# Performance work log

Measured on AMD Instinct MI355X. Metric: run time of the kernel, lower is better.

Reference implementation:

```python
import jax, jax.numpy as jnp
import numpy as np

N, IN_DIM, E, H, L, M = 65536, 512, 128, 4, 2, 256
DH = E // H  # 32

def _gaussian_orthogonal(m, d, rng):
    # FAVOR+ gaussian orthogonal random matrix (performer_pytorch, scaling=0)
    blocks = []
    for _ in range((m + d - 1) // d):
        q, _ = np.linalg.qr(rng.normal(size=(d, d)))
        blocks.append(q.T)
    mat = np.concatenate(blocks)[:m]
    mult = np.linalg.norm(rng.normal(size=(m, d)), axis=1)
    return (mult[:, None] * mat).astype(np.float32)

def setup_inputs() -> dict:
    rng = np.random.default_rng(0)
    r = lambda *s: jnp.asarray(rng.normal(size=s, scale=0.02), jnp.float32)
    z = lambda *s: jnp.zeros(s, jnp.float32)
    o = lambda *s: jnp.ones(s, jnp.float32)
    return dict(
        x=jnp.asarray(rng.normal(size=(N, IN_DIM)), dtype=jnp.float32),
        Wpin=r(IN_DIM, E), bpin=z(E),
        lag=o(L, E), lab=z(L, E),                    # performer inner pre-LN (attn)
        Wq=r(L, E, E), Wk=r(L, E, E), Wv=r(L, E, E), # qkv (no bias in performer_pytorch)
        Wo=r(L, E, E), bo=z(L, E),                   # attn to_out
        lbg=o(L, E), lbb=z(L, E),                    # performer inner pre-LN (ff)
        Wf1=r(L, E, 4 * E), bf1=z(L, 4 * E),         # performer inner GELU FFN
        Wf2=r(L, 4 * E, E), bf2=z(L, E),
        Wpo=r(L, E, E), bpo=z(L, E),                 # PerformerSelfAttention.out_proj
        n1g=o(L, E), n1b=z(L, E),                    # block norm1
        Wn1=r(L, E, 4 * E), bn1=z(L, 4 * E),         # block ReLU FFN
        Wn2=r(L, 4 * E, E), bn2=z(L, E),
        n2g=o(L, E), n2b=z(L, E),                    # block norm2
        Wc=r(E, 1), bc=z(1),                         # classifier
        proj=jnp.stack([jnp.asarray(_gaussian_orthogonal(M, DH, rng)) for _ in range(L)]),
    )

def _ln(x, g, b, eps=1e-5):
    mu = x.mean(-1, keepdims=True)
    var = ((x - mu) ** 2).mean(-1, keepdims=True)
    return (x - mu) * jax.lax.rsqrt(var + eps) * g + b

def _softmax_kernel(data, proj, is_query, eps=1e-4):
    # data: [1,H,N,DH]; proj: [M,DH]  (performer_pytorch softmax_kernel)
    dn = data.shape[-1] ** -0.25
    ratio = proj.shape[0] ** -0.5
    dd = jnp.einsum('bhnd,md->bhnm', data * dn, proj)
    diag = (data ** 2).sum(-1, keepdims=True) * 0.5 * (dn * dn)
    stab = jnp.max(dd, -1, keepdims=True) if is_query else jnp.max(dd)
    return ratio * (jnp.exp(dd - diag - stab) + eps)

def _linear_attn(qf, kf, v):
    # non-causal FAVOR+: O(N*M*DH)
    D = jnp.einsum('bhnm,bhm->bhn', qf, kf.sum(-2))          # denominator
    ctx = jnp.einsum('bhnm,bhnd->bhmd', kf, v)               # [1,H,M,DH]
    return jnp.einsum('bhnm,bhmd->bhnd', qf, ctx) / D[..., None]

def _forward(x, Wpin, bpin, lag, lab, Wq, Wk, Wv, Wo, bo, lbg, lbb,
             Wf1, bf1, Wf2, bf2, Wpo, bpo, n1g, n1b, Wn1, bn1, Wn2, bn2,
             n2g, n2b, Wc, bc, proj):
    h = (x @ Wpin + bpin)[None]  # [1,N,E]
    split = lambda t: t.reshape(1, -1, H, DH).transpose(0, 2, 1, 3)
    for l in range(L):
        # --- inner Performer (depth=1): pre-LN attn + pre-LN GELU FFN, residuals ---
        y = _ln(h, lag[l], lab[l])
        q, k, v = split(y @ Wq[l]), split(y @ Wk[l]), split(y @ Wv[l])
        qf = _softmax_kernel(q, proj[l], True)
        kf = _softmax_kernel(k, proj[l], False)
        a = _linear_attn(qf, kf, v).transpose(0, 2, 1, 3).reshape(1, -1, E)
        h1 = h + (a @ Wo[l] + bo[l])
        y2 = _ln(h1, lbg[l], lbb[l])
        h2 = h1 + (jax.nn.gelu(y2 @ Wf1[l] + bf1[l], approximate=False) @ Wf2[l] + bf2[l])
        # --- outer block: post-LN residual attn + post-LN ReLU FFN ---
        attn_out = h2 @ Wpo[l] + bpo[l]
        h = _ln(h + attn_out, n1g[l], n1b[l])
        ffn = jax.nn.relu(h @ Wn1[l] + bn1[l]) @ Wn2[l] + bn2[l]
        h = _ln(h + ffn, n2g[l], n2b[l])
    return jax.nn.sigmoid(h[0] @ Wc + bc)[:, 0]  # [N]

def reference(x, Wpin, bpin, lag, lab, Wq, Wk, Wv, Wo, bo, lbg, lbb,
              Wf1, bf1, Wf2, bf2, Wpo, bpo, n1g, n1b, Wn1, bn1, Wn2, bn2,
              n2g, n2b, Wc, bc, proj):
    return _forward(x, Wpin, bpin, lag, lab, Wq, Wk, Wv, Wo, bo, lbg, lbb,
                    Wf1, bf1, Wf2, bf2, Wpo, bpo, n1g, n1b, Wn1, bn1, Wn2, bn2,
                    n2g, n2b, Wc, bc, proj)
```

## Files before the change

kernel.cpp:

```cpp
#include <hip/hip_runtime.h>
#include <math.h>

#define NTOK  65536
#define EDIM  128
#define HN    4
#define DHD   32
#define MF    256
#define LLAYERS 2
#define INDIM 512
#define FDIM  512
#define CR    512
#define NCHK  (NTOK/CR)

#define DN    0.4204482076268573f
#define DN2   0.17677669529663687f
#define KEPS  1e-4f

typedef unsigned short u16;
typedef unsigned int   u32;
typedef __attribute__((ext_vector_type(8))) __bf16 bf16x8;
typedef __attribute__((ext_vector_type(4))) float  f32x4;

__device__ __forceinline__ u16 f2bf(float f){
  u32 u = __float_as_uint(f);
  u32 r = (u + 0x7fffu + ((u >> 16) & 1u)) >> 16;
  return (u16)r;
}
__device__ __forceinline__ float bf2f(u16 h){ return __uint_as_float(((u32)h) << 16); }

__device__ __forceinline__ void gload_lds16(const void* g, void* l){
  __builtin_amdgcn_global_load_lds(
      (const __attribute__((address_space(1))) u32*)g,
      (__attribute__((address_space(3))) u32*)l, 16, 0, 0);
}

__device__ __forceinline__ unsigned f2ord(float f){
  unsigned u = __float_as_uint(f);
  return (u & 0x80000000u) ? ~u : (u | 0x80000000u);
}
__device__ __forceinline__ float ord2f(unsigned e){
  unsigned u = (e & 0x80000000u) ? (e & 0x7fffffffu) : ~e;
  return __uint_as_float(u);
}

struct PrepArgs {
  const float* Wpin; const float* Wq; const float* Wk; const float* Wv;
  const float* Wo;   const float* Wpo; const float* Wf1; const float* Wf2;
  const float* Wn1;  const float* Wn2; const float* proj;
};

__global__ __launch_bounds__(256) void prep_kernel(PrepArgs a, u16* __restrict__ wts,
                                                   u16* __restrict__ pjb,
                                                   unsigned* __restrict__ stabp)
{
  int idx = blockIdx.x * 256 + threadIdx.x;
  if (idx == 0) { stabp[0] = 0x007FFFFFu; stabp[1] = 0x007FFFFFu; }
  const float* sp; u16* dp; int r, K, J;
  if      (idx <  65536) { sp = a.Wpin; dp = wts;          r = idx;          K = 512; J = 128; }
  else if (idx <  98304) { sp = a.Wq;   dp = wts +  65536; r = idx -  65536; K = 128; J = 128; }
  else if (idx < 131072) { sp = a.Wk;   dp = wts +  98304; r = idx -  98304; K = 128; J = 128; }
  else if (idx < 163840) { sp = a.Wv;   dp = wts + 131072; r = idx - 131072; K = 128; J = 128; }
  else if (idx < 196608) { sp = a.Wo;   dp = wts + 163840; r = idx - 163840; K = 128; J = 128; }
  else if (idx < 229376) { sp = a.Wpo;  dp = wts + 196608; r = idx - 196608; K = 128; J = 128; }
  else if (idx < 360448) { sp = a.Wf1;  dp = wts + 229376; r = idx - 229376; K = 128; J = 512; }
  else if (idx < 491520) { sp = a.Wf2;  dp = wts + 360448; r = idx - 360448; K = 512; J = 128; }
  else if (idx < 622592) { sp = a.Wn1;  dp = wts + 491520; r = idx - 491520; K = 128; J = 512; }
  else if (idx < 753664) { sp = a.Wn2;  dp = wts + 622592; r = idx - 622592; K = 512; J = 128; }
  else { int p = idx - 753664; pjb[p] = f2bf(a.proj[p] * DN); return; }
  int kj = K * J;
  int l = r / kj, rr = r - l * kj;
  int j = rr / K, k = rr - j * K;
  dp[r] = f2bf(sp[(size_t)l * kj + (size_t)k * J + j]);
}

template<int LNM, bool A32, bool MULTI>
__global__ __launch_bounds__(256, 4) void gemm_f(
    const u16* __restrict__ A, const float* __restrict__ Af,
    const u16* __restrict__ Bt,
    const float* __restrict__ bias, const u16* __restrict__ res,
    u16* __restrict__ outRaw, int K, int J, int op,
    const float* __restrict__ g1, const float* __restrict__ b1, u16* __restrict__ outL1,
    u16* __restrict__ outAux,
    const float* __restrict__ Wcp, const float* __restrict__ bcp, float* __restrict__ outCls)
{
  __shared__ __align__(16) u16 pool[18432];
  __shared__ float lnred[2][2][32][2];
  u16* Al = pool;
  u16* Bl = pool + 6144;
  const int tid  = threadIdx.x;
  const int lane = tid & 63;
  const int w    = tid >> 6;
  const int wr   = w >> 1, wc = w & 1;
  const int bid  = blockIdx.x;
  const int nwg8 = gridDim.x >> 3;
  const int bsw  = (bid & 7) * nwg8 + (bid >> 3);
  const int n0   = bsw * 64;
  const int jb   = MULTI ? 0 : blockIdx.y * 128;
  const u16* Bu  = MULTI ? (Bt + (size_t)blockIdx.y * 32768) : Bt;

  f32x4 acc[2][4];
#pragma unroll
  for (int m = 0; m < 2; ++m)
#pragma unroll
    for (int n = 0; n < 4; ++n) acc[m][n] = (f32x4){0.f, 0.f, 0.f, 0.f};

  const int srow = lane >> 2;
  const int skg  = (lane & 3) ^ ((lane >> 3) & 3);

  auto stageB = [&](int buf, int k0) {
#pragma unroll
    for (int i = 0; i < 2; ++i) {
      const int rb = 2 * w + i;
      gload_lds16(Bu + (size_t)(jb + rb * 16 + srow) * K + k0 + skg * 8,
                  &Bl[buf * 4096 + rb * 512]);
    }
  };
  auto stageA16 = [&](int buf, int k0) {
    gload_lds16(A + (size_t)(n0 + w * 16 + srow) * K + k0 + skg * 8,
                &Al[buf * 2048 + w * 512]);
  };

  const int r16f = lane & 15;
  const int kgl  = (lane >> 4) ^ ((lane >> 1) & 3);
  const int foff = r16f * 32 + kgl * 8;

  auto compute = [&](int cur) {
    bf16x8 af[2], bfg[4];
#pragma unroll
    for (int m = 0; m < 2; ++m)
      af[m]  = *reinterpret_cast<const bf16x8*>(&Al[cur * 2048 + (wr * 2 + m) * 512 + foff]);
#pragma unroll
    for (int n = 0; n < 4; ++n)
      bfg[n] = *reinterpret_cast<const bf16x8*>(&Bl[cur * 4096 + (wc * 4 + n) * 512 + foff]);
#pragma unroll
    for (int m = 0; m < 2; ++m)
#pragma unroll
      for (int n = 0; n < 4; ++n)
        acc[m][n] = __builtin_amdgcn_mfma_f32_16x16x32_bf16(af[m], bfg[n], acc[m][n], 0, 0, 0);
  };

  if constexpr (A32) {
    constexpr int T = 16;
    float4 fA[3][2];
    const int r = tid >> 2, hf = tid & 3;
    auto loadA = [&](int slot, int k0) {
      const float* gp = Af + (size_t)(n0 + r) * 512 + k0 + hf * 8;
      fA[slot][0] = ((const float4*)gp)[0];
      fA[slot][1] = ((const float4*)gp)[1];
    };
    const int rbA = r >> 4, r16A = r & 15, swzA = (r16A >> 1) & 3;
    auto writeA = [&](int slot, int buf) {
      uint4 p0;
      p0.x = (u32)f2bf(fA[slot][0].x) | ((u32)f2bf(fA[slot][0].y) << 16);
      p0.y = (u32)f2bf(fA[slot][0].z) | ((u32)f2bf(fA[slot][0].w) << 16);
      p0.z = (u32)f2bf(fA[slot][1].x) | ((u32)f2bf(fA[slot][1].y) << 16);
      p0.w = (u32)f2bf(fA[slot][1].z) | ((u32)f2bf(fA[slot][1].w) << 16);
      *reinterpret_cast<uint4*>(&Al[buf * 2048 + rbA * 512 + r16A * 32 + (hf ^ swzA) * 8]) = p0;
    };
    loadA(0, 0); loadA(1, 32); loadA(2, 64);
    stageB(0, 0); stageB(1, 32);
    asm volatile("s_waitcnt vmcnt(8)" ::: "memory");
    writeA(0, 0);
#pragma unroll
    for (int t = 0; t < T; ++t) {
      if (t + 2 < T) asm volatile("s_waitcnt vmcnt(4) lgkmcnt(0)" ::: "memory");
      else           asm volatile("s_waitcnt vmcnt(0) lgkmcnt(0)" ::: "memory");
      __builtin_amdgcn_s_barrier();
      if (t + 1 < T) writeA((t + 1) % 3, (t + 1) % 3);
      if (t + 3 < T) loadA((t + 3) % 3, (t + 3) * 32);
      if (t + 2 < T) stageB((t + 2) % 3, (t + 2) * 32);
      compute(t % 3);
    }
    __builtin_amdgcn_s_barrier();
  } else {
    const int T = K >> 5;
    stageA16(0, 0); stageB(0, 0);
    stageA16(1, 32); stageB(1, 32);
    for (int t = 0; t < T; ++t) {
      if (t + 1 < T) asm volatile("s_waitcnt vmcnt(3) lgkmcnt(0)" ::: "memory");
      else           asm volatile("s_waitcnt vmcnt(0) lgkmcnt(0)" ::: "memory");
      __builtin_amdgcn_s_barrier();
      int cur = t % 3;
      if (t + 2 < T) { stageA16((t + 2) % 3, (t + 2) * 32); stageB((t + 2) % 3, (t + 2) * 32); }
      compute(cur);
    }
    __builtin_amdgcn_s_barrier();
  }

  const int colb = jb + wc * 64 + (lane & 15);
  const int rowb = n0 + wr * 32 + (lane >> 4) * 4;
  float bv[4];
#pragma unroll
  for (int n = 0; n < 4; ++n) bv[n] = bias ? bias[colb + n * 16] : 0.f;

  float v[2][4][4];
#pragma unroll
  for (int m = 0; m < 2; ++m)
#pragma unroll
    for (int n = 0; n < 4; ++n)
#pragma unroll
      for (int j = 0; j < 4; ++j) {
        float t = acc[m][n][j] + bv[n];
        if (res) t += bf2f(res[(size_t)(rowb + m * 16 + j) * J + colb + n * 16]);
        v[m][n][j] = t;
      }

  if constexpr (MULTI) {
    if (blockIdx.y == 2) {
      u16* tb = pool;
#pragma unroll
      for (int m = 0; m < 2; ++m)
#pragma unroll
        for (int n = 0; n < 4; ++n)
#pragma unroll
          for (int j = 0; j < 4; ++j)
            tb[(wc * 64 + n * 16 + (lane & 15)) * 72 + wr * 32 + m * 16 + (lane >> 4) * 4 + j]
                = f2bf(v[m][n][j]);
      __syncthreads();
      { const int c2 = tid >> 1, hf2 = tid & 1;
        const uint4* src = reinterpret_cast<const uint4*>(&tb[c2 * 72 + hf2 * 32]);
        uint4* dst = reinterpret_cast<uint4*>(outAux + (size_t)c2 * NTOK + n0 + hf2 * 32);
        dst[0] = src[0]; dst[1] = src[1]; dst[2] = src[2]; dst[3] = src[3]; }
      return;
    }
    u16* out0 = (blockIdx.y == 0) ? outRaw : outL1;
#pragma unroll
    for (int m = 0; m < 2; ++m)
#pragma unroll
      for (int n = 0; n < 4; ++n)
#pragma unroll
        for (int j = 0; j < 4; ++j)
          out0[(size_t)(rowb + m * 16 + j) * J + colb + n * 16] = f2bf(v[m][n][j]);
    return;
  }

  if (outRaw) {
#pragma unroll
    for (int m = 0; m < 2; ++m)
#pragma unroll
      for (int n = 0; n < 4; ++n)
#pragma unroll
        for (int j = 0; j < 4; ++j)
          outRaw[(size_t)(rowb + m * 16 + j) * J + colb + n * 16] = f2bf(v[m][n][j]);
  }

  if constexpr (LNM > 0 && !MULTI) {
    float rs[2][4], rq[2][4];
#pragma unroll
    for (int m = 0; m < 2; ++m)
#pragma unroll
      for (int j = 0; j < 4; ++j) {
        float s = 0.f, q = 0.f;
#pragma unroll
        for (int n = 0; n < 4; ++n) { float t = v[m][n][j]; s += t; q += t * t; }
        rs[m][j] = s; rq[m][j] = q;
      }
#pragma unroll
    for (int o = 1; o < 16; o <<= 1)
#pragma unroll
      for (int m = 0; m < 2; ++m)
#pragma unroll
        for (int j = 0; j < 4; ++j) {
          rs[m][j] += __shfl_xor(rs[m][j], o);
          rq[m][j] += __shfl_xor(rq[m][j], o);
        }
    __syncthreads();
    if ((lane & 15) == 0) {
#pragma unroll
      for (int m = 0; m < 2; ++m)
#pragma unroll
        for (int j = 0; j < 4; ++j) {
          int rloc = m * 16 + (lane >> 4) * 4 + j;
          lnred[wr][wc][rloc][0] = rs[m][j];
          lnred[wr][wc][rloc][1] = rq[m][j];
        }
    }
    __syncthreads();
    float gg[4], bb[4];
#pragma unroll
    for (int n = 0; n < 4; ++n) { gg[n] = g1[colb + n * 16]; bb[n] = b1[colb + n * 16]; }
#pragma unroll
    for (int m = 0; m < 2; ++m)
#pragma unroll
      for (int j = 0; j < 4; ++j) {
        int rloc = m * 16 + (lane >> 4) * 4 + j;
        float ts = rs[m][j] + lnred[wr][wc ^ 1][rloc][0];
        float tq = rq[m][j] + lnred[wr][wc ^ 1][rloc][1];
        float mu = ts * (1.f / 128.f);
        float rsig = rsqrtf(tq * (1.f / 128.f) - mu * mu + 1e-5f);
#pragma unroll
        for (int n = 0; n < 4; ++n)
          v[m][n][j] = (v[m][n][j] - mu) * rsig * gg[n] + bb[n];
      }
    if (outL1) {
#pragma unroll
      for (int m = 0; m < 2; ++m)
#pragma unroll
        for (int n = 0; n < 4; ++n)
#pragma unroll
          for (int j = 0; j < 4; ++j)
            outL1[(size_t)(rowb + m * 16 + j) * J + colb + n * 16] = f2bf(v[m][n][j]);
    }
  }
}

template<bool RESPOST, int ACT, int LNM>
__global__ __launch_bounds__(256, 2) void mega_f(
    const u16* __restrict__ A0, const u16* __restrict__ W0t,
    const float* __restrict__ b0p, const u16* __restrict__ res0,
    const float* __restrict__ g0, const float* __restrict__ bg0,
    const u16* __restrict__ W1t, const float* __restrict__ fb1p,
    const u16* __restrict__ W2t, const float* __restrict__ fb2p,
    u16* __restrict__ out,
    const float* __restrict__ g1, const float* __restrict__ bt1,
    u16* __restrict__ outL2, const float* __restrict__ g2, const float* __restrict__ bt2,
    const float* __restrict__ Wcp, const float* __restrict__ bcp, float* __restrict__ outCls)
{
  __shared__ __align__(16) u16 As[4][2048];
  __shared__ __align__(16) u16 Hs[4][2048];
  __shared__ __align__(16) u16 Bs[3][4096];
  __shared__ float lnred[2][2][32][2];
  const int tid  = threadIdx.x;
  const int lane = tid & 63;
  const int w    = tid >> 6;
  const int wr   = w >> 1, wc = w & 1;
  const int bid  = blockIdx.x;
  const int bsw  = (bid & 7) * (gridDim.x >> 3) + (bid >> 3);
  const int n0   = bsw * 64;

  const int srow = lane >> 2;
  const int skg  = (lane & 3) ^ ((lane >> 3) & 3);
  const int r16f = lane & 15;
  const int kgl  = (lane >> 4) ^ ((lane >> 1) & 3);
  const int foff = r16f * 32 + kgl * 8;
  const int colb = wc * 64 + (lane & 15);
  const int rowb = n0 + wr * 32 + (lane >> 4) * 4;

#pragma unroll
  for (int rb = 0; rb < 4; ++rb)
    gload_lds16(A0 + (size_t)(n0 + rb * 16 + srow) * EDIM + w * 32 + skg * 8, &As[w][rb * 512]);

  auto stageB = [&](int buf, int st) {
    const u16* base; size_t rstride; int kb0;
    if (st < 4) { base = W0t; rstride = 128; kb0 = st * 32; }
    else {
      int s2 = st - 4;
      int c = s2 >> 3, p = (s2 >> 2) & 1, kt = s2 & 3;
      if (p == 0) { base = W1t + (size_t)c * 16384; rstride = 128; kb0 = kt * 32; }
      else        { base = W2t;                      rstride = 512; kb0 = c * 128 + kt * 32; }
    }
#pragma unroll
    for (int i = 0; i < 2; ++i) {
      const int rb = 2 * w + i;
      gload_lds16(base + (size_t)(rb * 16 + srow) * rstride + kb0 + skg * 8, &Bs[buf][rb * 512]);
    }
  };

  stageB(0, 0);
  stageB(1, 1);

  f32x4 acc0[2][4], acc1[2][4], acc2[2][4];
#pragma unroll
  for (int m = 0; m < 2; ++m)
#pragma unroll
    for (int n = 0; n < 4; ++n) { acc0[m][n] = (f32x4){0.f,0.f,0.f,0.f}; acc2[m][n] = (f32x4){0.f,0.f,0.f,0.f}; }

  float v0[2][4][4];

#pragma unroll
  for (int st = 0; st < 36; ++st) {
    if (st + 1 < 36) asm volatile("s_waitcnt vmcnt(2) lgkmcnt(0)" ::: "memory");
    else             asm volatile("s_waitcnt vmcnt(0) lgkmcnt(0)" ::: "memory");
    __builtin_amdgcn_s_barrier();
    if (st + 2 < 36) stageB((st + 2) % 3, st + 2);

    if (st < 4) {
      const u16* Bc = &Bs[st % 3][0];
      bf16x8 af[2], bfg[4];
#pragma unroll
      for (int m = 0; m < 2; ++m) af[m]  = *reinterpret_cast<const bf16x8*>(&As[st][(wr * 2 + m) * 512 + foff]);
#pragma unroll
      for (int n = 0; n < 4; ++n) bfg[n] = *reinterpret_cast<const bf16x8*>(&Bc[(wc * 4 + n) * 512 + foff]);
#pragma unroll
      for (int m = 0; m < 2; ++m)
#pragma unroll
        for (int n = 0; n < 4; ++n)
          acc0[m][n] = __builtin_amdgcn_mfma_f32_16x16x32_bf16(af[m], bfg[n], acc0[m][n], 0, 0, 0);
      if (st == 3) {
        float bv0[4];
#pragma unroll
        for (int n = 0; n < 4; ++n) bv0[n] = b0p[colb + n * 16];
#pragma unroll
        for (int m = 0; m < 2; ++m)
#pragma unroll
          for (int n = 0; n < 4; ++n)
#pragma unroll
            for (int j = 0; j < 4; ++j)
              v0[m][n][j] = acc0[m][n][j] + bv0[n]
                  + bf2f(res0[(size_t)(rowb + m * 16 + j) * EDIM + colb + n * 16]);
        float rs[2][4], rq[2][4];
#pragma unroll
        for (int m = 0; m < 2; ++m)
#pragma unroll
          for (int j = 0; j < 4; ++j) {
            float s = 0.f, q = 0.f;
#pragma unroll
            for (int n = 0; n < 4; ++n) { float t = v0[m][n][j]; s += t; q += t * t; }
            rs[m][j] = s; rq[m][j] = q;
          }
#pragma unroll
        for (int o = 1; o < 16; o <<= 1)
#pragma unroll
          for (int m = 0; m < 2; ++m)
#pragma unroll
            for (int j = 0; j < 4; ++j) {
              rs[m][j] += __shfl_xor(rs[m][j], o);
              rq[m][j] += __shfl_xor(rq[m][j], o);
            }
        __syncthreads();
        if ((lane & 15) == 0) {
#pragma unroll
          for (int m = 0; m < 2; ++m)
#pragma unroll
            for (int j = 0; j < 4; ++j) {
              int rloc = m * 16 + (lane >> 4) * 4 + j;
              lnred[wr][wc][rloc][0] = rs[m][j];
              lnred[wr][wc][rloc][1] = rq[m][j];
            }
        }
        __syncthreads();
        float gg[4], bb[4];
#pragma unroll
        for (int n = 0; n < 4; ++n) { gg[n] = g0[colb + n * 16]; bb[n] = bg0[colb + n * 16]; }
#pragma unroll
        for (int m = 0; m < 2; ++m)
#pragma unroll
          for (int j = 0; j < 4; ++j) {
            int rloc = m * 16 + (lane >> 4) * 4 + j;
            float ts = rs[m][j] + lnred[wr][wc ^ 1][rloc][0];
            float tq = rq[m][j] + lnred[wr][wc ^ 1][rloc][1];
            float mu = ts * (1.f / 128.f);
            float rsig = rsqrtf(tq * (1.f / 128.f) - mu * mu + 1e-5f);
            const int r16 = (lane >> 4) * 4 + j;
            const int rb  = wr * 2 + m;
#pragma unroll
            for (int n = 0; n < 4; ++n) {
              float lnv = (v0[m][n][j] - mu) * rsig * gg[n] + bb[n];
              const int q = wc * 64 + n * 16 + (lane & 15);
              const int ts2 = q >> 5, ql = q & 31;
              const int s = (ql >> 3) ^ ((r16 >> 1) & 3);
              As[ts2][rb * 512 + r16 * 32 + s * 8 + (ql & 7)] = f2bf(lnv);
              if (RESPOST) v0[m][n][j] = lnv;
            }
          }
      }
    } else {
      const int s2 = st - 4;
      const int c = s2 >> 3, p = (s2 >> 2) & 1, kt = s2 & 3;
      if ((s2 & 7) == 0) {
#pragma unroll
        for (int m = 0; m < 2; ++m)
#pragma unroll
          for (int n = 0; n < 4; ++n) acc1[m][n] = (f32x4){0.f, 0.f, 0.f, 0.f};
      }
      const u16* Asrc = p ? &Hs[kt][0] : &As[kt][0];
      const u16* Bc = &Bs[st % 3][0];
      bf16x8 af[2], bfg[4];
#pragma unroll
      for (int m = 0; m < 2; ++m) af[m]  = *reinterpret_cast<const bf16x8*>(&Asrc[(wr * 2 + m) * 512 + foff]);
#pragma unroll
      for (int n = 0; n < 4; ++n) bfg[n] = *reinterpret_cast<const bf16x8*>(&Bc[(wc * 4 + n) * 512 + foff]);
      if (p == 0) {
#pragma unroll
        for (int m = 0; m < 2; ++m)
#pragma unroll
          for (int n = 0; n < 4; ++n)
            acc1[m][n] = __builtin_amdgcn_mfma_f32_16x16x32_bf16(af[m], bfg[n], acc1[m][n], 0, 0, 0);
      } else {
#pragma unroll
        for (int m = 0; m < 2; ++m)
#pragma unroll
          for (int n = 0; n < 4; ++n)
            acc2[m][n] = __builtin_amdgcn_mfma_f32_16x16x32_bf16(af[m], bfg[n], acc2[m][n], 0, 0, 0);
      }
      if ((s2 & 7) == 3) {
        float fb[4];
#pragma unroll
        for (int n = 0; n < 4; ++n) fb[n] = fb1p[c * 128 + wc * 64 + n * 16 + (lane & 15)];
#pragma unroll
        for (int m = 0; m < 2; ++m)
#pragma unroll
          for (int n = 0; n < 4; ++n)
#pragma unroll
            for (int j = 0; j < 4; ++j) {
              float t = acc1[m][n][j] + fb[n];
              if (ACT == 1) t = 0.5f * t * (1.f + erff(t * 0.70710678118654752f));
              else          t = fmaxf(t, 0.f);
              const int r16 = (lane >> 4) * 4 + j;
              const int rb  = wr * 2 + m;
              const int q   = wc * 64 + n * 16 + (lane & 15);
              const int ts2 = q >> 5, ql = q & 31;
              const int s   = (ql >> 3) ^ ((r16 >> 1) & 3);
              Hs[ts2][rb * 512 + r16 * 32 + s * 8 + (ql & 7)] = f2bf(t);
            }
      }
    }
  }

  float fb[4];
#pragma unroll
  for (int n = 0; n < 4; ++n) fb[n] = fb2p[colb + n * 16];
  float v[2][4][4];
#pragma unroll
  for (int m = 0; m < 2; ++m)
#pragma unroll
    for (int n = 0; n < 4; ++n)
#pragma unroll
      for (int j = 0; j < 4; ++j)
        v[m][n][j] = acc2[m][n][j] + fb[n] + v0[m][n][j];

  auto ln_apply = [&](const float* gp, const float* bp) {
    float rs[2][4], rq[2][4];
#pragma unroll
    for (int m = 0; m < 2; ++m)
#pragma unroll
      for (int j = 0; j < 4; ++j) {
        float s = 0.f, q = 0.f;
#pragma unroll
        for (int n = 0; n < 4; ++n) { float t = v[m][n][j]; s += t; q += t * t; }
        rs[m][j] = s; rq[m][j] = q;
      }
#pragma unroll
    for (int o = 1; o < 16; o <<= 1)
#pragma unroll
      for (int m = 0; m < 2; ++m)
#pragma unroll
        for (int j = 0; j < 4; ++j) {
          rs[m][j] += __shfl_xor(rs[m][j], o);
          rq[m][j] += __shfl_xor(rq[m][j], o);
        }
    __syncthreads();
    if ((lane & 15) == 0) {
#pragma unroll
      for (int m = 0; m < 2; ++m)
#pragma unroll
        for (int j = 0; j < 4; ++j) {
          int rloc = m * 16 + (lane >> 4) * 4 + j;
          lnred[wr][wc][rloc][0] = rs[m][j];
          lnred[wr][wc][rloc][1] = rq[m][j];
        }
    }
    __syncthreads();
    float gg[4], bb[4];
#pragma unroll
    for (int n = 0; n < 4; ++n) { gg[n] = gp[colb + n * 16]; bb[n] = bp[colb + n * 16]; }
#pragma unroll
    for (int m = 0; m < 2; ++m)
#pragma unroll
      for (int j = 0; j < 4; ++j) {
        int rloc = m * 16 + (lane >> 4) * 4 + j;
        float ts = rs[m][j] + lnred[wr][wc ^ 1][rloc][0];
        float tq = rq[m][j] + lnred[wr][wc ^ 1][rloc][1];
        float mu = ts * (1.f / 128.f);
        float rsig = rsqrtf(tq * (1.f / 128.f) - mu * mu + 1e-5f);
#pragma unroll
        for (int n = 0; n < 4; ++n)
          v[m][n][j] = (v[m][n][j] - mu) * rsig * gg[n] + bb[n];
      }
  };

  if constexpr (LNM > 0) ln_apply(g1, bt1);
#pragma unroll
  for (int m = 0; m < 2; ++m)
#pragma unroll
    for (int n = 0; n < 4; ++n)
#pragma unroll
      for (int j = 0; j < 4; ++j)
        out[(size_t)(rowb + m * 16 + j) * EDIM + colb + n * 16] = f2bf(v[m][n][j]);

  if constexpr (LNM == 2) {
    ln_apply(g2, bt2);
#pragma unroll
    for (int m = 0; m < 2; ++m)
#pragma unroll
      for (int n = 0; n < 4; ++n)
#pragma unroll
        for (int j = 0; j < 4; ++j)
          outL2[(size_t)(rowb + m * 16 + j) * EDIM + colb + n * 16] = f2bf(v[m][n][j]);
  }
  if constexpr (LNM == 3) {
    const float bc0 = bcp[0];
    float wv[4];
#pragma unroll
    for (int n = 0; n < 4; ++n) wv[n] = Wcp[colb + n * 16];
    float dp[2][4];
#pragma unroll
    for (int m = 0; m < 2; ++m)
#pragma unroll
      for (int j = 0; j < 4; ++j) {
        float s = 0.f;
#pragma unroll
        for (int n = 0; n < 4; ++n) s += v[m][n][j] * wv[n];
        dp[m][j] = s;
      }
#pragma unroll
    for (int o = 1; o < 16; o <<= 1)
#pragma unroll
      for (int m = 0; m < 2; ++m)
#pragma unroll
        for (int j = 0; j < 4; ++j) dp[m][j] += __shfl_xor(dp[m][j], o);
    __syncthreads();
    if ((lane & 15) == 0) {
#pragma unroll
      for (int m = 0; m < 2; ++m)
#pragma unroll
        for (int j = 0; j < 4; ++j)
          lnred[wr][wc][m * 16 + (lane >> 4) * 4 + j][0] = dp[m][j];
    }
    __syncthreads();
    if (wc == 0 && (lane & 15) == 0) {
#pragma unroll
      for (int m = 0; m < 2; ++m)
#pragma unroll
        for (int j = 0; j < 4; ++j) {
          int rloc = m * 16 + (lane >> 4) * 4 + j;
          float t = dp[m][j] + lnred[wr][1][rloc][0] + bc0;
          outCls[n0 + wr * 32 + rloc] = 1.f / (1.f + expf(-t));
        }
    }
  }
}

__global__ __launch_bounds__(256) void smax_kernel(
    const u16* __restrict__ Km, const u16* __restrict__ pjb,
    unsigned* __restrict__ stabp)
{
  __shared__ float wred[4];
  const int tid = threadIdx.x, lane = tid & 63, w = tid >> 6;
  const int h = blockIdx.y;
  const int n0 = blockIdx.x * 256 + w * 64;
  const int g = lane >> 4, c = lane & 15;
  bf16x8 af[4];
#pragma unroll
  for (int mf = 0; mf < 4; ++mf)
    af[mf] = *reinterpret_cast<const bf16x8*>(
        Km + (size_t)(n0 + mf * 16 + c) * EDIM + h * DHD + g * 8);
  float lm = -3.4e38f;
  const f32x4 z = (f32x4){0.f, 0.f, 0.f, 0.f};
#pragma unroll
  for (int jf = 0; jf < 16; ++jf) {
    bf16x8 bfg = *reinterpret_cast<const bf16x8*>(pjb + (jf * 16 + c) * DHD + g * 8);
#pragma unroll
    for (int mf = 0; mf < 4; ++mf) {
      f32x4 d = __builtin_amdgcn_mfma_f32_16x16x32_bf16(af[mf], bfg, z, 0, 0, 0);
      lm = fmaxf(lm, fmaxf(fmaxf(d[0], d[1]), fmaxf(d[2], d[3])));
    }
  }
#pragma unroll
  for (int o = 1; o < 64; o <<= 1) lm = fmaxf(lm, __shfl_xor(lm, o));
  if (lane == 0) wred[w] = lm;
  __syncthreads();
  if (tid == 0)
    atomicMax(stabp, f2ord(fmaxf(fmaxf(wred[0], wred[1]), fmaxf(wred[2], wred[3]))));
}

__global__ __launch_bounds__(256) void ctxk_kernel(
    const u16* __restrict__ Km, const u16* __restrict__ VT,
    const u16* __restrict__ pjb, const unsigned* __restrict__ stabp,
    float* __restrict__ pctx, float* __restrict__ pks)
{
  __shared__ __align__(16) u16 kfT[256 * 40];
  const int tid = threadIdx.x, lane = tid & 63, w = tid >> 6;
  const int h = blockIdx.y, ch = blockIdx.x;
  const int n0 = ch * CR;
  const int g = lane >> 4, c = lane & 15;
  const float stab = ord2f(*stabp);
  const f32x4 z = (f32x4){0.f, 0.f, 0.f, 0.f};

  bf16x8 pf[4];
#pragma unroll
  for (int jf = 0; jf < 4; ++jf)
    pf[jf] = *reinterpret_cast<const bf16x8*>(pjb + ((w * 4 + jf) * 16 + c) * DHD + g * 8);

  f32x4 cacc[4][2];
#pragma unroll
  for (int mf = 0; mf < 4; ++mf)
#pragma unroll
    for (int df = 0; df < 2; ++df) cacc[mf][df] = z;
  float ksacc[4] = {0.f, 0.f, 0.f, 0.f};

  for (int s = 0; s < CR / 32; ++s) {
    const int rbase = n0 + s * 32;
    bf16x8 af[2];
    float s2[2];
#pragma unroll
    for (int rf = 0; rf < 2; ++rf) {
      af[rf] = *reinterpret_cast<const bf16x8*>(
          Km + (size_t)(rbase + rf * 16 + c) * EDIM + h * DHD + g * 8);
      uint4 ui = *reinterpret_cast<const uint4*>(&af[rf]);
      u32 wd[4] = {ui.x, ui.y, ui.z, ui.w};
      float ss = 0.f;
#pragma unroll
      for (int i = 0; i < 4; ++i) {
        float a = bf2f((u16)(wd[i] & 0xffff)), b = bf2f((u16)(wd[i] >> 16));
        ss += a * a + b * b;
      }
      ss += __shfl_xor(ss, 16); ss += __shfl_xor(ss, 32);
      s2[rf] = ss;
    }
#pragma unroll
    for (int rf = 0; rf < 2; ++rf) {
      float dg[4];
#pragma unroll
      for (int r = 0; r < 4; ++r)
        dg[r] = 0.5f * DN2 * __shfl(s2[rf], (lane & 48) | (4 * g + r)) + stab;
#pragma unroll
      for (int jf = 0; jf < 4; ++jf) {
        f32x4 d = __builtin_amdgcn_mfma_f32_16x16x32_bf16(af[rf], pf[jf], z, 0, 0, 0);
        u16 b0 = f2bf(__expf(d[0] - dg[0]) + KEPS);
        u16 b1 = f2bf(__expf(d[1] - dg[1]) + KEPS);
        u16 b2 = f2bf(__expf(d[2] - dg[2]) + KEPS);
        u16 b3 = f2bf(__expf(d[3] - dg[3]) + KEPS);
        uint2 pk;
        pk.x = (u32)b0 | ((u32)b1 << 16);
        pk.y = (u32)b2 | ((u32)b3 << 16);
        *reinterpret_cast<uint2*>(&kfT[(size_t)(w * 64 + jf * 16 + c) * 40 + rf * 16 + 4 * g]) = pk;
        ksacc[jf] += bf2f(b0) + bf2f(b1) + bf2f(b2) + bf2f(b3);
      }
    }
#pragma unroll
    for (int mf = 0; mf < 4; ++mf) {
      bf16x8 a = *reinterpret_cast<const bf16x8*>(&kfT[(size_t)(w * 64 + mf * 16 + c) * 40 + g * 8]);
#pragma unroll
      for (int df = 0; df < 2; ++df) {
        bf16x8 b = *reinterpret_cast<const bf16x8*>(
            VT + (size_t)(h * DHD + df * 16 + c) * NTOK + rbase + g * 8);
        cacc[mf][df] = __builtin_amdgcn_mfma_f32_16x16x32_bf16(a, b, cacc[mf][df], 0, 0, 0);
      }
    }
  }
#pragma unroll
  for (int jf = 0; jf < 4; ++jf) {
    float vv = ksacc[jf];
    vv += __shfl_xor(vv, 16); vv += __shfl_xor(vv, 32);
    if (g == 0) pks[((size_t)h * NCHK + ch) * MF + w * 64 + jf * 16 + c] = vv;
  }
#pragma unroll
  for (int mf = 0; mf < 4; ++mf)
#pragma unroll
    for (int df = 0; df < 2; ++df)
#pragma unroll
      for (int r = 0; r < 4; ++r) {
        int m = w * 64 + mf * 16 + 4 * g + r;
        int d = df * 16 + c;
        pctx[(((size_t)h * NCHK + ch) * MF + m) * DHD + d] = cacc[mf][df][r];
      }
}

__global__ __launch_bounds__(256) void reduce_all(
    const float* __restrict__ pctx, const float* __restrict__ pks,
    u16* __restrict__ ctxT, float* __restrict__ ksg)
{
  int idx = blockIdx.x * 256 + threadIdx.x;
  if (idx < HN * MF * DHD) {
    int h = idx >> 13, md = idx & 8191;
    int m = md >> 5, d = md & 31;
    float s = 0.f;
    for (int c = 0; c < NCHK; ++c) s += pctx[((size_t)h * NCHK + c) * 8192 + md];
    ctxT[(size_t)h * 8192 + d * MF + m] = f2bf(s);
  } else {
    int i2 = idx - HN * MF * DHD;
    if (i2 < HN * MF) {
      int h = i2 >> 8, m = i2 & 255;
      float s = 0.f;
      for (int c = 0; c < NCHK; ++c) s += pks[((size_t)h * NCHK + c) * MF + m];
      ksg[i2] = s;
    }
  }
}

__global__ __launch_bounds__(256) void qout_kernel(
    const u16* __restrict__ Qm, const u16* __restrict__ pjb,
    const u16* __restrict__ ctxT, const float* __restrict__ ksg,
    u16* __restrict__ Am)
{
  __shared__ __align__(16) u16 qfs[4][32 * 40];
  const int tid = threadIdx.x, lane = tid & 63, w = tid >> 6;
  const int h = blockIdx.y;
  const int n0 = blockIdx.x * 128 + w * 32;
  const int g = lane >> 4, c = lane & 15;
  const f32x4 z = (f32x4){0.f, 0.f, 0.f, 0.f};

  bf16x8 af[2];
  float s2[2];
#pragma unroll
  for (int rf = 0; rf < 2; ++rf) {
    af[rf] = *reinterpret_cast<const bf16x8*>(
        Qm + (size_t)(n0 + rf * 16 + c) * EDIM + h * DHD + g * 8);
    uint4 ui = *reinterpret_cast<const uint4*>(&af[rf]);
    u32 wd[4] = {ui.x, ui.y, ui.z, ui.w};
    float ss = 0.f;
#pragma unroll
    for (int i = 0; i < 4; ++i) {
      float a = bf2f((u16)(wd[i] & 0xffff)), b = bf2f((u16)(wd[i] >> 16));
      ss += a * a + b * b;
    }
    ss += __shfl_xor(ss, 16); ss += __shfl_xor(ss, 32);
    s2[rf] = ss;
  }

  float rmax[2][4];
#pragma unroll
  for (int rf = 0; rf < 2; ++rf)
#pragma unroll
    for (int r = 0; r < 4; ++r) rmax[rf][r] = -3.4e38f;
#pragma unroll
  for (int jf = 0; jf < 16; ++jf) {
    bf16x8 b = *reinterpret_cast<const bf16x8*>(pjb + (jf * 16 + c) * DHD + g * 8);
#pragma unroll
    for (int rf = 0; rf < 2; ++rf) {
      f32x4 d = __builtin_amdgcn_mfma_f32_16x16x32_bf16(af[rf], b, z, 0, 0, 0);
#pragma unroll
      for (int r = 0; r < 4; ++r) rmax[rf][r] = fmaxf(rmax[rf][r], d[r]);
    }
  }
#pragma unroll
  for (int rf = 0; rf < 2; ++rf)
#pragma unroll
    for (int r = 0; r < 4; ++r) {
      float vv = rmax[rf][r];
      vv = fmaxf(vv, __shfl_xor(vv, 1)); vv = fmaxf(vv, __shfl_xor(vv, 2));
      vv = fmaxf(vv, __shfl_xor(vv, 4)); vv = fmaxf(vv, __shfl_xor(vv, 8));
      rmax[rf][r] = vv;
    }
  float crow[2][4];
#pragma unroll
  for (int rf = 0; rf < 2; ++rf)
#pragma unroll
    for (int r = 0; r < 4; ++r)
      crow[rf][r] = 0.5f * DN2 * __shfl(s2[rf], (lane & 48) | (4 * g + r)) + rmax[rf][r];

  f32x4 oacc[2][2];
#pragma unroll
  for (int rf = 0; rf < 2; ++rf)
#pragma unroll
    for (int df = 0; df < 2; ++df) oacc[rf][df] = z;
  float Dacc[2][4];
#pragma unroll
  for (int rf = 0; rf < 2; ++rf)
#pragma unroll
    for (int r = 0; r < 4; ++r) Dacc[rf][r] = 0.f;

  for (int ks = 0; ks < 8; ++ks) {
#pragma unroll
    for (int jj = 0; jj < 2; ++jj) {
      const int jf = ks * 2 + jj;
      bf16x8 b = *reinterpret_cast<const bf16x8*>(pjb + (jf * 16 + c) * DHD + g * 8);
      const float ksv = ksg[h * MF + jf * 16 + c];
#pragma unroll
      for (int rf = 0; rf < 2; ++rf) {
        f32x4 d = __builtin_amdgcn_mfma_f32_16x16x32_bf16(af[rf], b, z, 0, 0, 0);
#pragma unroll
        for (int r = 0; r < 4; ++r) {
          float q = __expf(d[r] - crow[rf][r]) + KEPS;
          u16 qb_ = f2bf(q);
          qfs[w][(rf * 16 + 4 * g + r) * 40 + jj * 16 + c] = qb_;
          Dacc[rf][r] += bf2f(qb_) * ksv;
        }
      }
    }
#pragma unroll
    for (int rf = 0; rf < 2; ++rf) {
      bf16x8 a = *reinterpret_cast<const bf16x8*>(&qfs[w][(rf * 16 + c) * 40 + g * 8]);
#pragma unroll
      for (int df = 0; df < 2; ++df) {
        bf16x8 bc = *reinterpret_cast<const bf16x8*>(
            ctxT + (size_t)(h * DHD + df * 16 + c) * MF + ks * 32 + g * 8);
        oacc[rf][df] = __builtin_amdgcn_mfma_f32_16x16x32_bf16(a, bc, oacc[rf][df], 0, 0, 0);
      }
    }
  }
#pragma unroll
  for (int rf = 0; rf < 2; ++rf)
#pragma unroll
    for (int r = 0; r < 4; ++r) {
      float vv = Dacc[rf][r];
      vv += __shfl_xor(vv, 1); vv += __shfl_xor(vv, 2);
      vv += __shfl_xor(vv, 4); vv += __shfl_xor(vv, 8);
      Dacc[rf][r] = vv;
    }
#pragma unroll
  for (int rf = 0; rf < 2; ++rf)
#pragma unroll
    for (int df = 0; df < 2; ++df)
#pragma unroll
      for (int r = 0; r < 4; ++r)
        Am[(size_t)(n0 + rf * 16 + 4 * g + r) * EDIM + h * DHD + df * 16 + c] =
            f2bf(oacc[rf][df][r] / Dacc[rf][r]);
}

extern "C" void kernel_launch(void* const* d_in, const int* in_sizes, int n_in,
                              void* d_out, int out_size, void* d_ws, size_t ws_size,
                              hipStream_t stream)
{
  const float* x    = (const float*)d_in[0];
  const float* Wpin = (const float*)d_in[1];
  const float* bpin = (const float*)d_in[2];
  const float* lag  = (const float*)d_in[3];
  const float* lab  = (const float*)d_in[4];
  const float* Wq   = (const float*)d_in[5];
  const float* Wk   = (const float*)d_in[6];
  const float* Wv   = (const float*)d_in[7];
  const float* Wo   = (const float*)d_in[8];
  const float* bo   = (const float*)d_in[9];
  const float* lbg  = (const float*)d_in[10];
  const float* lbb  = (const float*)d_in[11];
  const float* Wf1  = (const float*)d_in[12];
  const float* bf1  = (const float*)d_in[13];
  const float* Wf2  = (const float*)d_in[14];
  const float* bf2  = (const float*)d_in[15];
  const float* Wpo  = (const float*)d_in[16];
  const float* bpo  = (const float*)d_in[17];
  const float* n1g  = (const float*)d_in[18];
  const float* n1b  = (const float*)d_in[19];
  const float* Wn1  = (const float*)d_in[20];
  const float* bn1  = (const float*)d_in[21];
  const float* Wn2  = (const float*)d_in[22];
  const float* bn2  = (const float*)d_in[23];
  const float* n2g  = (const float*)d_in[24];
  const float* n2b  = (const float*)d_in[25];
  const float* Wc   = (const float*)d_in[26];
  const float* bc   = (const float*)d_in[27];
  const float* proj = (const float*)d_in[28];

  size_t off = 0;
  char* base = (char*)d_ws;
  auto alloc = [&](size_t bytes) -> void* {
    void* p = base + off;
    off += (bytes + 255) & ~(size_t)255;
    return p;
  };
  u16* hb  = (u16*)alloc((size_t)NTOK * EDIM * 2);
  u16* yb  = (u16*)alloc((size_t)NTOK * EDIM * 2);
  u16* qb  = (u16*)alloc((size_t)NTOK * EDIM * 2);
  u16* kb  = (u16*)alloc((size_t)NTOK * EDIM * 2);
  u16* vb  = (u16*)alloc((size_t)NTOK * EDIM * 2);
  u16* VT  = (u16*)alloc((size_t)HN * DHD * NTOK * 2);
  u16* pjb = (u16*)alloc((size_t)LLAYERS * MF * DHD * 2);
  u16* ctxT = (u16*)alloc((size_t)HN * DHD * MF * 2);
  float* ksg  = (float*)alloc((size_t)HN * MF * 4);
  float* pctx = (float*)alloc((size_t)HN * NCHK * MF * DHD * 4);
  float* pks  = (float*)alloc((size_t)HN * NCHK * MF * 4);
  unsigned* stabp = (unsigned*)alloc(256);
  u16* wts = (u16*)alloc((size_t)753664 * 2);

  u16* Wpint = wts;
  auto Wqt  = [&](int l){ return wts +  65536 + (size_t)l * 16384; };
  auto Wot  = [&](int l){ return wts + 163840 + (size_t)l * 16384; };
  auto Wpot = [&](int l){ return wts + 196608 + (size_t)l * 16384; };
  auto Wf1t = [&](int l){ return wts + 229376 + (size_t)l * 65536; };
  auto Wf2t = [&](int l){ return wts + 360448 + (size_t)l * 65536; };
  auto Wn1t = [&](int l){ return wts + 491520 + (size_t)l * 65536; };
  auto Wn2t = [&](int l){ return wts + 622592 + (size_t)l * 65536; };

  PrepArgs pa{Wpin, Wq, Wk, Wv, Wo, Wpo, Wf1, Wf2, Wn1, Wn2, proj};
  prep_kernel<<<3008, 256, 0, stream>>>(pa, wts, pjb, stabp);

  gemm_f<1, true, false><<<dim3(NTOK / 64, 1), 256, 0, stream>>>(
      nullptr, x, Wpint, bpin, nullptr, hb, INDIM, EDIM, 0,
      lag, lab, yb, nullptr, nullptr, nullptr, nullptr);

  for (int l = 0; l < LLAYERS; ++l) {
    const u16* pjl = pjb + (size_t)l * MF * DHD;

    gemm_f<0, false, true><<<dim3(NTOK / 64, 3), 256, 0, stream>>>(
        yb, nullptr, Wqt(l), nullptr, nullptr, qb, EDIM, EDIM, 0,
        nullptr, nullptr, kb, VT, nullptr, nullptr, nullptr);

    smax_kernel<<<dim3(NTOK / 256, HN), 256, 0, stream>>>(kb, pjl, stabp + l);
    ctxk_kernel<<<dim3(NCHK, HN), 256, 0, stream>>>(kb, VT, pjl, stabp + l, pctx, pks);
    reduce_all<<<132, 256, 0, stream>>>(pctx, pks, ctxT, ksg);
    qout_kernel<<<dim3(NTOK / 128, HN), 256, 0, stream>>>(qb, pjl, ctxT, ksg, yb);

    mega_f<false, 1, 0><<<NTOK / 64, 256, 0, stream>>>(
        yb, Wot(l), bo + l * EDIM, hb, lbg + l * EDIM, lbb + l * EDIM,
        Wf1t(l), bf1 + l * FDIM, Wf2t(l), bf2 + l * EDIM, vb,
        nullptr, nullptr, nullptr, nullptr, nullptr, nullptr, nullptr, nullptr);

    if (l < LLAYERS - 1) {
      mega_f<true, 2, 2><<<NTOK / 64, 256, 0, stream>>>(
          vb, Wpot(l), bpo + l * EDIM, hb, n1g + l * EDIM, n1b + l * EDIM,
          Wn1t(l), bn1 + l * FDIM, Wn2t(l), bn2 + l * EDIM, hb,
          n2g + l * EDIM, n2b + l * EDIM,
          yb, lag + (l + 1) * EDIM, lab + (l + 1) * EDIM,
          nullptr, nullptr, nullptr);
    } else {
      mega_f<true, 2, 3><<<NTOK / 64, 256, 0, stream>>>(
          vb, Wpot(l), bpo + l * EDIM, hb, n1g + l * EDIM, n1b + l * EDIM,
          Wn1t(l), bn1 + l * FDIM, Wn2t(l), bn2 + l * EDIM, hb,
          n2g + l * EDIM, n2b + l * EDIM,
          nullptr, nullptr, nullptr,
          Wc, bc, (float*)d_out);
    }
  }
}
```

Before: 514.8 us.

## Fuse key-feature max into ctx pass and apply stabilizer in reduction

Eliminates the separate max-reduction kernel over key projections by computing per-chunk maxima inside the context accumulation kernel. The global stabilizer is factored out as a scale exp(-stab) applied during the final reduction, with the epsilon term reconstructed from per-chunk value sums and token count. This saves a full pass over K with MFMA work and an atomic, at the risk of overflow since exponentials are no longer max-shifted before bf16 rounding.

```diff
diff --git a/kernel.cpp b/kernel.cpp
--- a/kernel.cpp
+++ b/kernel.cpp
@@ -34,15 +34,6 @@
       (__attribute__((address_space(3))) u32*)l, 16, 0, 0);
 }
 
-__device__ __forceinline__ unsigned f2ord(float f){
-  unsigned u = __float_as_uint(f);
-  return (u & 0x80000000u) ? ~u : (u | 0x80000000u);
-}
-__device__ __forceinline__ float ord2f(unsigned e){
-  unsigned u = (e & 0x80000000u) ? (e & 0x7fffffffu) : ~e;
-  return __uint_as_float(u);
-}
-
 struct PrepArgs {
   const float* Wpin; const float* Wq; const float* Wk; const float* Wv;
   const float* Wo;   const float* Wpo; const float* Wf1; const float* Wf2;
@@ -50,11 +41,9 @@
 };
 
 __global__ __launch_bounds__(256) void prep_kernel(PrepArgs a, u16* __restrict__ wts,
-                                                   u16* __restrict__ pjb,
-                                                   unsigned* __restrict__ stabp)
+                                                   u16* __restrict__ pjb)
 {
   int idx = blockIdx.x * 256 + threadIdx.x;
-  if (idx == 0) { stabp[0] = 0x007FFFFFu; stabp[1] = 0x007FFFFFu; }
   const float* sp; u16* dp; int r, K, J;
   if      (idx <  65536) { sp = a.Wpin; dp = wts;          r = idx;          K = 512; J = 128; }
   else if (idx <  98304) { sp = a.Wq;   dp = wts +  65536; r = idx -  65536; K = 128; J = 128; }
@@ -631,50 +620,18 @@
   }
 }
 
-__global__ __launch_bounds__(256) void smax_kernel(
-    const u16* __restrict__ Km, const u16* __restrict__ pjb,
-    unsigned* __restrict__ stabp)
-{
-  __shared__ float wred[4];
-  const int tid = threadIdx.x, lane = tid & 63, w = tid >> 6;
-  const int h = blockIdx.y;
-  const int n0 = blockIdx.x * 256 + w * 64;
-  const int g = lane >> 4, c = lane & 15;
-  bf16x8 af[4];
-#pragma unroll
-  for (int mf = 0; mf < 4; ++mf)
-    af[mf] = *reinterpret_cast<const bf16x8*>(
-        Km + (size_t)(n0 + mf * 16 + c) * EDIM + h * DHD + g * 8);
-  float lm = -3.4e38f;
-  const f32x4 z = (f32x4){0.f, 0.f, 0.f, 0.f};
-#pragma unroll
-  for (int jf = 0; jf < 16; ++jf) {
-    bf16x8 bfg = *reinterpret_cast<const bf16x8*>(pjb + (jf * 16 + c) * DHD + g * 8);
-#pragma unroll
-    for (int mf = 0; mf < 4; ++mf) {
-      f32x4 d = __builtin_amdgcn_mfma_f32_16x16x32_bf16(af[mf], bfg, z, 0, 0, 0);
-      lm = fmaxf(lm, fmaxf(fmaxf(d[0], d[1]), fmaxf(d[2], d[3])));
-    }
-  }
-#pragma unroll
-  for (int o = 1; o < 64; o <<= 1) lm = fmaxf(lm, __shfl_xor(lm, o));
-  if (lane == 0) wred[w] = lm;
-  __syncthreads();
-  if (tid == 0)
-    atomicMax(stabp, f2ord(fmaxf(fmaxf(wred[0], wred[1]), fmaxf(wred[2], wred[3]))));
-}
-
 __global__ __launch_bounds__(256) void ctxk_kernel(
     const u16* __restrict__ Km, const u16* __restrict__ VT,
-    const u16* __restrict__ pjb, const unsigned* __restrict__ stabp,
-    float* __restrict__ pctx, float* __restrict__ pks)
+    const u16* __restrict__ pjb,
+    float* __restrict__ pctx, float* __restrict__ pks,
+    float* __restrict__ pvs, float* __restrict__ pmax)
 {
   __shared__ __align__(16) u16 kfT[256 * 40];
+  __shared__ float wred[4];
   const int tid = threadIdx.x, lane = tid & 63, w = tid >> 6;
   const int h = blockIdx.y, ch = blockIdx.x;
   const int n0 = ch * CR;
   const int g = lane >> 4, c = lane & 15;
-  const float stab = ord2f(*stabp);
   const f32x4 z = (f32x4){0.f, 0.f, 0.f, 0.f};
 
   bf16x8 pf[4];
@@ -688,6 +645,8 @@
 #pragma unroll
     for (int df = 0; df < 2; ++df) cacc[mf][df] = z;
   float ksacc[4] = {0.f, 0.f, 0.f, 0.f};
+  float lm = -3.4e38f;
+  float vs[2] = {0.f, 0.f};
 
   for (int s = 0; s < CR / 32; ++s) {
     const int rbase = n0 + s * 32;
@@ -713,14 +672,15 @@
       float dg[4];
 #pragma unroll
       for (int r = 0; r < 4; ++r)
-        dg[r] = 0.5f * DN2 * __shfl(s2[rf], (lane & 48) | (4 * g + r)) + stab;
+        dg[r] = 0.5f * DN2 * __shfl(s2[rf], (lane & 48) | (4 * g + r));
 #pragma unroll
       for (int jf = 0; jf < 4; ++jf) {
         f32x4 d = __builtin_amdgcn_mfma_f32_16x16x32_bf16(af[rf], pf[jf], z, 0, 0, 0);
-        u16 b0 = f2bf(__expf(d[0] - dg[0]) + KEPS);
-        u16 b1 = f2bf(__expf(d[1] - dg[1]) + KEPS);
-        u16 b2 = f2bf(__expf(d[2] - dg[2]) + KEPS);
-        u16 b3 = f2bf(__expf(d[3] - dg[3]) + KEPS);
+        lm = fmaxf(lm, fmaxf(fmaxf(d[0], d[1]), fmaxf(d[2], d[3])));
+        u16 b0 = f2bf(__expf(d[0] - dg[0]));
+        u16 b1 = f2bf(__expf(d[1] - dg[1]));
+        u16 b2 = f2bf(__expf(d[2] - dg[2]));
+        u16 b3 = f2bf(__expf(d[3] - dg[3]));
         uint2 pk;
         pk.x = (u32)b0 | ((u32)b1 << 16);
         pk.y = (u32)b2 | ((u32)b3 << 16);
@@ -738,6 +698,20 @@
         cacc[mf][df] = __builtin_amdgcn_mfma_f32_16x16x32_bf16(a, b, cacc[mf][df], 0, 0, 0);
       }
     }
+    if (w == 0) {
+#pragma unroll
+      for (int df = 0; df < 2; ++df) {
+        bf16x8 b = *reinterpret_cast<const bf16x8*>(
+            VT + (size_t)(h * DHD + df * 16 + c) * NTOK + rbase + g * 8);
+        uint4 ub = *reinterpret_cast<const uint4*>(&b);
+        u32 wd2[4] = {ub.x, ub.y, ub.z, ub.w};
+        float sv = 0.f;
+#pragma unroll
+        for (int i = 0; i < 4; ++i)
+          sv += bf2f((u16)(wd2[i] & 0xffff)) + bf2f((u16)(wd2[i] >> 16));
+        vs[df] += sv;
+      }
+    }
   }
 #pragma unroll
   for (int jf = 0; jf < 4; ++jf) {
@@ -755,26 +729,54 @@
         int d = df * 16 + c;
         pctx[(((size_t)h * NCHK + ch) * MF + m) * DHD + d] = cacc[mf][df][r];
       }
+  if (w == 0) {
+#pragma unroll
+    for (int df = 0; df < 2; ++df) {
+      float v2 = vs[df];
+      v2 += __shfl_xor(v2, 16); v2 += __shfl_xor(v2, 32);
+      if (g == 0) pvs[((size_t)h * NCHK + ch) * DHD + df * 16 + c] = v2;
+    }
+  }
+#pragma unroll
+  for (int o = 1; o < 64; o <<= 1) lm = fmaxf(lm, __shfl_xor(lm, o));
+  if (lane == 0) wred[w] = lm;
+  __syncthreads();
+  if (tid == 0)
+    pmax[h * NCHK + ch] = fmaxf(fmaxf(wred[0], wred[1]), fmaxf(wred[2], wred[3]));
 }
 
 __global__ __launch_bounds__(256) void reduce_all(
     const float* __restrict__ pctx, const float* __restrict__ pks,
+    const float* __restrict__ pvs, const float* __restrict__ pmax,
     u16* __restrict__ ctxT, float* __restrict__ ksg)
 {
-  int idx = blockIdx.x * 256 + threadIdx.x;
+  __shared__ float red[4];
+  const int tid = threadIdx.x;
+  float m = fmaxf(pmax[tid], pmax[tid + 256]);
+#pragma unroll
+  for (int o = 1; o < 64; o <<= 1) m = fmaxf(m, __shfl_xor(m, o));
+  if ((tid & 63) == 0) red[tid >> 6] = m;
+  __syncthreads();
+  const float stab = fmaxf(fmaxf(red[0], red[1]), fmaxf(red[2], red[3]));
+  const float esc = __expf(-stab);
+
+  int idx = blockIdx.x * 256 + tid;
   if (idx < HN * MF * DHD) {
     int h = idx >> 13, md = idx & 8191;
-    int m = md >> 5, d = md & 31;
-    float s = 0.f;
-    for (int c = 0; c < NCHK; ++c) s += pctx[((size_t)h * NCHK + c) * 8192 + md];
-    ctxT[(size_t)h * 8192 + d * MF + m] = f2bf(s);
+    int mm = md >> 5, d = md & 31;
+    float s = 0.f, vsum = 0.f;
+    for (int c = 0; c < NCHK; ++c) {
+      s    += pctx[((size_t)h * NCHK + c) * 8192 + md];
+      vsum += pvs[((size_t)h * NCHK + c) * DHD + d];
+    }
+    ctxT[(size_t)h * 8192 + d * MF + mm] = f2bf(esc * s + KEPS * vsum);
   } else {
     int i2 = idx - HN * MF * DHD;
     if (i2 < HN * MF) {
-      int h = i2 >> 8, m = i2 & 255;
+      int h = i2 >> 8, mm = i2 & 255;
       float s = 0.f;
-      for (int c = 0; c < NCHK; ++c) s += pks[((size_t)h * NCHK + c) * MF + m];
-      ksg[i2] = s;
+      for (int c = 0; c < NCHK; ++c) s += pks[((size_t)h * NCHK + c) * MF + mm];
+      ksg[i2] = esc * s + KEPS * (float)NTOK;
     }
   }
 }
@@ -951,7 +953,8 @@
   float* ksg  = (float*)alloc((size_t)HN * MF * 4);
   float* pctx = (float*)alloc((size_t)HN * NCHK * MF * DHD * 4);
   float* pks  = (float*)alloc((size_t)HN * NCHK * MF * 4);
-  unsigned* stabp = (unsigned*)alloc(256);
+  float* pvs  = (float*)alloc((size_t)HN * NCHK * DHD * 4);
+  float* pmax = (float*)alloc((size_t)HN * NCHK * 4);
   u16* wts = (u16*)alloc((size_t)753664 * 2);
 
   u16* Wpint = wts;
@@ -964,7 +967,7 @@
   auto Wn2t = [&](int l){ return wts + 622592 + (size_t)l * 65536; };
 
   PrepArgs pa{Wpin, Wq, Wk, Wv, Wo, Wpo, Wf1, Wf2, Wn1, Wn2, proj};
-  prep_kernel<<<3008, 256, 0, stream>>>(pa, wts, pjb, stabp);
+  prep_kernel<<<3008, 256, 0, stream>>>(pa, wts, pjb);
 
   gemm_f<1, true, false><<<dim3(NTOK / 64, 1), 256, 0, stream>>>(
       nullptr, x, Wpint, bpin, nullptr, hb, INDIM, EDIM, 0,
@@ -977,9 +980,8 @@
         yb, nullptr, Wqt(l), nullptr, nullptr, qb, EDIM, EDIM, 0,
         nullptr, nullptr, kb, VT, nullptr, nullptr, nullptr);
 
-    smax_kernel<<<dim3(NTOK / 256, HN), 256, 0, stream>>>(kb, pjl, stabp + l);
-    ctxk_kernel<<<dim3(NCHK, HN), 256, 0, stream>>>(kb, VT, pjl, stabp + l, pctx, pks);
-    reduce_all<<<132, 256, 0, stream>>>(pctx, pks, ctxT, ksg);
+    ctxk_kernel<<<dim3(NCHK, HN), 256, 0, stream>>>(kb, VT, pjl, pctx, pks, pvs, pmax);
+    reduce_all<<<132, 256, 0, stream>>>(pctx, pks, pvs, pmax, ctxT, ksg);
     qout_kernel<<<dim3(NTOK / 128, HN), 256, 0, stream>>>(qb, pjl, ctxT, ksg, yb);
 
     mega_f<false, 1, 0><<<NTOK / 64, 256, 0, stream>>>(
```

Result: faster. 471.4 us (-8.4%).
